# Optimization experiments

Hardware: AMD Instinct MI355X
Metric: run time of the kernel (lower is better)

Reference implementation:

```python
import jax, jax.numpy as jnp
import numpy as np

Q_HEADS = 16
KV_HEADS = 4
ROPE_THETA = 10000.0


def _rope(x, seq_len):
    # x: [B, S, H, D]; pairs are consecutive along D (view_as_complex semantics)
    D = x.shape[-1]
    inv_freq = 1.0 / (ROPE_THETA ** (jnp.arange(0, D, 2, dtype=jnp.float32) / D))
    freqs = jnp.arange(seq_len, dtype=jnp.float32)[:, None] * inv_freq  # [S, D/2]
    cos = jnp.cos(freqs)[None, :, None, :]
    sin = jnp.sin(freqs)[None, :, None, :]
    xr = x.reshape(x.shape[:-1] + (D // 2, 2))
    x0, x1 = xr[..., 0], xr[..., 1]
    out = jnp.stack([x0 * cos - x1 * sin, x0 * sin + x1 * cos], axis=-1)
    return out.reshape(x.shape)


def setup_inputs() -> dict:
    key = jax.random.key(0)
    ks = jax.random.split(key, 6)
    B, S, E = 1, 2048, 2048
    KV_DIM = KV_HEADS * (E // Q_HEADS)  # 512
    scale = 0.02
    return {
        "x": jax.random.normal(ks[0], (B, S, E), dtype=jnp.float32),
        "Wq": jax.random.normal(ks[1], (E, E), dtype=jnp.float32) * scale,
        "Wk": jax.random.normal(ks[2], (KV_DIM, E), dtype=jnp.float32) * scale,
        "Wv": jax.random.normal(ks[3], (KV_DIM, E), dtype=jnp.float32) * scale,
        "Wo": jax.random.normal(ks[4], (E, E), dtype=jnp.float32) * scale,
        "bo": jax.random.normal(ks[5], (E,), dtype=jnp.float32) * scale,
        "cache_keys": jnp.zeros((B, S, KV_HEADS, E // Q_HEADS), dtype=jnp.float32),
        "cache_value": jnp.zeros((B, S, KV_HEADS, E // Q_HEADS), dtype=jnp.float32),
        "start_pos": 0,
    }


def reference(x, Wq, Wk, Wv, Wo, bo, cache_keys, cache_value, start_pos):
    B, S, E = x.shape
    hd = E // Q_HEADS
    G = Q_HEADS // KV_HEADS  # queries per kv head

    xq = (x @ Wq.T).reshape(B, S, Q_HEADS, hd)
    xk = (x @ Wk.T).reshape(B, S, KV_HEADS, hd)
    xv = (x @ Wv.T).reshape(B, S, KV_HEADS, hd)

    # Original applies RoPE with positions 0..seq_len-1 for both q and k
    # (freq tensor is sliced [:seq_len] inside apply_rotry_position_embedding).
    xq = _rope(xq, S)
    xk = _rope(xk, S)

    # cache write at start_pos (static python int)
    cache_keys = jax.lax.dynamic_update_slice(cache_keys, xk, (0, start_pos, 0, 0))
    cache_value = jax.lax.dynamic_update_slice(cache_value, xv, (0, start_pos, 0, 0))
    total = start_pos + S
    k_full = cache_keys[:, :total]   # [B, T, KVH, hd]
    v_full = cache_value[:, :total]

    # repeat_interleave over the head axis == GQA expansion
    k = jnp.repeat(k_full, G, axis=2)  # [B, T, QH, hd]
    v = jnp.repeat(v_full, G, axis=2)

    scores = jnp.einsum("bshd,bthd->bhst", xq, k) / jnp.sqrt(jnp.float32(hd))
    causal = jnp.triu(jnp.ones((S, total), dtype=bool), k=1)  # [S, T]
    scores = jnp.where(causal[None, None, :, :], -jnp.inf, scores)
    weights = jax.nn.softmax(scores, axis=-1)
    out = jnp.einsum("bhst,bthd->bshd", weights, v).reshape(B, S, E)
    # dropout p=0.0 / eval mode -> identity
    return out @ Wo.T + bo
```

## Files before the change

### kernel.cpp

```cpp
#include <hip/hip_runtime.h>
#include <stdint.h>

typedef unsigned short u16;
typedef float  f32x4  __attribute__((ext_vector_type(4)));
typedef __bf16 bf16x8 __attribute__((ext_vector_type(8)));
typedef __bf16 bf16x4 __attribute__((ext_vector_type(4)));
typedef unsigned short u16x8 __attribute__((ext_vector_type(8)));
typedef unsigned short u16x4v __attribute__((ext_vector_type(4)));

#define S_LEN 2048
#define E_DIM 2048
#define HD    128
#define QH    16
#define KVH   4
#define KVD   512
#define NQKV  3072
#define QK_SCALE 0.08838834764831845f

#define AS1 __attribute__((address_space(1)))
#define AS3 __attribute__((address_space(3)))

__device__ __forceinline__ u16 f2bf(float f) {
  union { float f; uint32_t u; } v; v.f = f;
  return (u16)((v.u + 0x7FFFu + ((v.u >> 16) & 1u)) >> 16);
}

__global__ void cast_bf16_kernel(const float* __restrict__ in, u16* __restrict__ out) {
  int i = blockIdx.x * blockDim.x + threadIdx.x;
  float4 f = reinterpret_cast<const float4*>(in)[i];
  u16x4v o;
  o[0] = f2bf(f.x); o[1] = f2bf(f.y); o[2] = f2bf(f.z); o[3] = f2bf(f.w);
  reinterpret_cast<u16x4v*>(out)[i] = o;
}

template<bool BIAS>
__global__ __launch_bounds__(256) void gemm_bt_kernel(
    const u16* __restrict__ A, const u16* __restrict__ B,
    float* __restrict__ C, const float* __restrict__ bias,
    int M, int N, int K)
{
  __shared__ u16 As[2][128 * 64];
  __shared__ u16 Bs[2][128 * 64];

  const int tid  = threadIdx.x;
  const int lane = tid & 63;
  const int wid  = tid >> 6;
  const int wr   = (wid >> 1) * 64;
  const int wc   = (wid & 1) * 64;
  const int lr   = lane & 15;
  const int kg   = lane >> 4;

  const int bm = blockIdx.y * 128;
  const int bn = blockIdx.x * 128;

  f32x4 acc[4][4];
  #pragma unroll
  for (int r = 0; r < 4; ++r)
    #pragma unroll
    for (int c = 0; c < 4; ++c) acc[r][c] = (f32x4){0.f, 0.f, 0.f, 0.f};

  const int l8 = lane & 7;
  const int l3 = lane >> 3;
  const int schunk = l8 ^ l3;

  const u16* gA = A + (size_t)(bm + wid*32 + l3) * K + schunk * 8;
  const u16* gB = B + (size_t)(bn + wid*32 + l3) * K + schunk * 8;

  const int sw = lr & 7;

  auto stage = [&](int buf, int kt) {
    #pragma unroll
    for (int i = 0; i < 4; ++i) {
      __builtin_amdgcn_global_load_lds(
          (const AS1 void*)(gA + (size_t)i * 8 * K + kt),
          (AS3 void*)(&As[buf][wid*32*64 + i*8*64]), 16, 0, 0);
      __builtin_amdgcn_global_load_lds(
          (const AS1 void*)(gB + (size_t)i * 8 * K + kt),
          (AS3 void*)(&Bs[buf][wid*32*64 + i*8*64]), 16, 0, 0);
    }
  };

  stage(0, 0);
  __syncthreads();

  int cur = 0;
  for (int kt = 0; kt < K; kt += 64) {
    if (kt + 64 < K) stage(cur ^ 1, kt + 64);
    #pragma unroll
    for (int kk = 0; kk < 2; ++kk) {
      bf16x8 af[4], bfr[4];
      #pragma unroll
      for (int r = 0; r < 4; ++r)
        af[r] = *reinterpret_cast<const bf16x8*>(
            &As[cur][(wr + r*16 + lr)*64 + ((kk*4 + kg) ^ sw)*8]);
      #pragma unroll
      for (int c = 0; c < 4; ++c)
        bfr[c] = *reinterpret_cast<const bf16x8*>(
            &Bs[cur][(wc + c*16 + lr)*64 + ((kk*4 + kg) ^ sw)*8]);
      #pragma unroll
      for (int r = 0; r < 4; ++r)
        #pragma unroll
        for (int c = 0; c < 4; ++c)
          acc[r][c] = __builtin_amdgcn_mfma_f32_16x16x32_bf16(af[r], bfr[c], acc[r][c], 0, 0, 0);
    }
    __syncthreads();
    cur ^= 1;
  }

  const int crow = kg * 4;
  #pragma unroll
  for (int r = 0; r < 4; ++r) {
    #pragma unroll
    for (int c = 0; c < 4; ++c) {
      int gr = bm + wr + r*16 + crow;
      int gc = bn + wc + c*16 + lr;
      float badd = BIAS ? bias[gc] : 0.0f;
      #pragma unroll
      for (int reg = 0; reg < 4; ++reg)
        C[(size_t)(gr + reg)*N + gc] = acc[r][c][reg] + badd;
    }
  }
}

__global__ void rope_split_kernel(const float* __restrict__ qkv,
                                  u16* __restrict__ qb, u16* __restrict__ kb) {
  int idx = blockIdx.x * blockDim.x + threadIdx.x;
  int s  = idx / 1280;
  int cp = idx - s * 1280;
  int col = cp * 2;
  const float* src = qkv + (size_t)s * NQKV + col;
  float x0 = src[0], x1 = src[1];
  int p = (col & 127) >> 1;
  float inv = exp2f((float)p * (-13.287712379549449f / 64.0f));
  float ang = (float)s * inv;
  float sn, cs;
  sincosf(ang, &sn, &cs);
  float o0 = x0 * cs - x1 * sn;
  float o1 = x0 * sn + x1 * cs;
  if (col < E_DIM) {
    o0 *= QK_SCALE; o1 *= QK_SCALE;
    qb[(size_t)s * E_DIM + col]     = f2bf(o0);
    qb[(size_t)s * E_DIM + col + 1] = f2bf(o1);
  } else {
    kb[(size_t)s * KVD + (col - E_DIM)]     = f2bf(o0);
    kb[(size_t)s * KVD + (col - E_DIM) + 1] = f2bf(o1);
  }
}

__global__ void transpose_v_kernel(const float* __restrict__ qkv, u16* __restrict__ vT) {
  __shared__ float tile[32][33];
  const int sbase = blockIdx.x * 32;
  const int cbase = blockIdx.y * 32;
  const int tx = threadIdx.x;
  const int ty = threadIdx.y;
  #pragma unroll
  for (int i = 0; i < 32; i += 8)
    tile[ty + i][tx] = qkv[(size_t)(sbase + ty + i) * NQKV + (E_DIM + KVD) + cbase + tx];
  __syncthreads();
  #pragma unroll
  for (int i = 0; i < 32; i += 8)
    vT[(size_t)(cbase + ty + i) * S_LEN + sbase + tx] = f2bf(tile[tx][ty + i]);
}

__device__ __forceinline__ void attn_tile(
    int t, int qt, int wid, int lr, int kg,
    const bf16x8* qf, f32x4* o, float& mr, float& ls,
    const u16* ks, const u16* vts, u16* ps)
{
  const int sw = lr & 7;
  f32x4 st[4];
  #pragma unroll
  for (int c = 0; c < 4; ++c) st[c] = (f32x4){0.f, 0.f, 0.f, 0.f};
  __builtin_amdgcn_s_setprio(1);
  #pragma unroll
  for (int kk = 0; kk < 4; ++kk) {
    #pragma unroll
    for (int c = 0; c < 4; ++c) {
      bf16x8 kfr = *reinterpret_cast<const bf16x8*>(
          &ks[(c*16 + lr)*128 + ((kk*4 + kg) ^ sw)*8]);
      st[c] = __builtin_amdgcn_mfma_f32_16x16x32_bf16(kfr, qf[kk], st[c], 0, 0, 0);
    }
  }
  __builtin_amdgcn_s_setprio(0);
  if (t == qt) {
    #pragma unroll
    for (int c = 0; c < 4; ++c)
      #pragma unroll
      for (int reg = 0; reg < 4; ++reg)
        if (c*16 + kg*4 + reg > wid*16 + lr) st[c][reg] = -1e30f;
  }
  float cm[4];
  #pragma unroll
  for (int c = 0; c < 4; ++c)
    cm[c] = fmaxf(fmaxf(st[c][0], st[c][1]), fmaxf(st[c][2], st[c][3]));
  float pm = fmaxf(fmaxf(cm[0], cm[1]), fmaxf(cm[2], cm[3]));
  pm = fmaxf(pm, __shfl_xor(pm, 16));
  pm = fmaxf(pm, __shfl_xor(pm, 32));

  if (!__all(pm - mr <= 8.0f)) {
    float nm = fmaxf(mr, pm);
    float alpha = __expf(mr - nm);
    ls *= alpha;
    mr = nm;
    float ar[4];
    #pragma unroll
    for (int reg = 0; reg < 4; ++reg)
      ar[reg] = __shfl(alpha, kg*4 + reg);
    #pragma unroll
    for (int d = 0; d < 8; ++d)
      #pragma unroll
      for (int reg = 0; reg < 4; ++reg)
        o[d][reg] *= ar[reg];
  }

  float p[4][4];
  float csum[4];
  #pragma unroll
  for (int c = 0; c < 4; ++c) {
    #pragma unroll
    for (int reg = 0; reg < 4; ++reg)
      p[c][reg] = __expf(st[c][reg] - mr);
    csum[c] = (p[c][0] + p[c][1]) + (p[c][2] + p[c][3]);
  }
  float sum = (csum[0] + csum[1]) + (csum[2] + csum[3]);
  sum += __shfl_xor(sum, 16);
  sum += __shfl_xor(sum, 32);
  ls += sum;

  #pragma unroll
  for (int c = 0; c < 4; ++c) {
    bf16x4 pk;
    #pragma unroll
    for (int reg = 0; reg < 4; ++reg) pk[reg] = (__bf16)p[c][reg];
    *reinterpret_cast<bf16x4*>(&ps[lr*72 + c*16 + kg*4]) = pk;
  }
  __builtin_amdgcn_s_setprio(1);
  #pragma unroll
  for (int kk = 0; kk < 2; ++kk) {
    bf16x8 pa = *reinterpret_cast<const bf16x8*>(&ps[lr*72 + kk*32 + kg*8]);
    #pragma unroll
    for (int d = 0; d < 8; ++d) {
      bf16x8 vb = *reinterpret_cast<const bf16x8*>(
          &vts[(d*16 + lr)*64 + ((kk*4 + kg) ^ sw)*8]);
      o[d] = __builtin_amdgcn_mfma_f32_16x16x32_bf16(pa, vb, o[d], 0, 0, 0);
    }
  }
  __builtin_amdgcn_s_setprio(0);
}

__global__ __launch_bounds__(256, 2) void attn_kernel(
    const u16* __restrict__ Q, const u16* __restrict__ Kc,
    const u16* __restrict__ VT, u16* __restrict__ Out)
{
  __shared__ u16 Ks[2][64 * 128];
  __shared__ u16 VTs[2][128 * 64];
  __shared__ u16 Ps[4][16 * 72];

  const int x = blockIdx.x;
  int qt, h;
  if (x < 256) { qt = x & 31; h = x >> 5; }
  else         { int xp = x - 256; qt = 31 - (xp & 31); h = 8 + (xp >> 5); }
  const int kvh = h >> 2;
  const int tid  = threadIdx.x;
  const int lane = tid & 63;
  const int wid  = tid >> 6;
  const int lr   = lane & 15;
  const int kg   = lane >> 4;

  const int NT = qt + 1;

  bf16x8 qf[4];
  {
    const u16* qa = Q + (size_t)(qt*64 + wid*16 + lr) * E_DIM + h * HD + kg * 8;
    #pragma unroll
    for (int kk = 0; kk < 4; ++kk)
      qf[kk] = *reinterpret_cast<const bf16x8*>(qa + kk * 32);
  }

  f32x4 o[8];
  #pragma unroll
  for (int d = 0; d < 8; ++d) o[d] = (f32x4){0.f,0.f,0.f,0.f};
  float mr = -1e30f, ls = 0.f;

  u16x8 kreg[4], vreg[4];
  const u16* kbase = Kc + kvh * HD;
  const u16* vbase = VT + (size_t)(kvh * HD) * S_LEN;

  auto stage_load = [&](int t) {
    #pragma unroll
    for (int i = 0; i < 4; ++i) {
      int c = i * 256 + tid;
      kreg[i] = *reinterpret_cast<const u16x8*>(
          kbase + (size_t)(t*64 + (c >> 4)) * KVD + (c & 15) * 8);
      vreg[i] = *reinterpret_cast<const u16x8*>(
          vbase + (size_t)(c >> 3) * S_LEN + t*64 + (c & 7) * 8);
    }
  };
  auto stage_write = [&](int b) {
    #pragma unroll
    for (int i = 0; i < 4; ++i) {
      int c = i * 256 + tid;
      int kr = c >> 4, kc = c & 15;
      *reinterpret_cast<u16x8*>(&Ks[b][kr*128 + (kc ^ (kr & 7))*8]) = kreg[i];
      int vr = c >> 3, vc = c & 7;
      *reinterpret_cast<u16x8*>(&VTs[b][vr*64 + (vc ^ (vr & 7))*8]) = vreg[i];
    }
  };

  int p = 0;
  stage_load(0);
  stage_write(0);
  __syncthreads();

  for (int t = 0; t < NT; ++t) {
    if (t + 1 < NT) stage_load(t + 1);
    attn_tile(t, qt, wid, lr, kg, qf, o, mr, ls, Ks[p], VTs[p], Ps[wid]);
    if (t + 1 < NT) {
      stage_write(p ^ 1);
      __syncthreads();
      p ^= 1;
    }
  }

  {
    float inv = 1.0f / ls;
    float ivq[4];
    #pragma unroll
    for (int reg = 0; reg < 4; ++reg)
      ivq[reg] = __shfl(inv, kg*4 + reg);
    #pragma unroll
    for (int reg = 0; reg < 4; ++reg) {
      int grow = qt*64 + wid*16 + kg*4 + reg;
      #pragma unroll
      for (int d = 0; d < 8; ++d)
        Out[(size_t)grow * E_DIM + h * HD + d*16 + lr] =
            __builtin_bit_cast(u16, (__bf16)(o[d][reg] * ivq[reg]));
    }
  }
}

extern "C" void kernel_launch(void* const* d_in, const int* in_sizes, int n_in,
                              void* d_out, int out_size, void* d_ws, size_t ws_size,
                              hipStream_t stream)
{
  const float* x  = (const float*)d_in[0];
  const float* Wq = (const float*)d_in[1];
  const float* Wk = (const float*)d_in[2];
  const float* Wv = (const float*)d_in[3];
  const float* Wo = (const float*)d_in[4];
  const float* bo = (const float*)d_in[5];
  float* out = (float*)d_out;

  char* w = (char*)d_ws;
  u16*   xb   = (u16*)(w);
  u16*   Wcat = (u16*)(w + (8u  << 20));
  u16*   Wob  = (u16*)(w + (20u << 20));
  float* qkv  = (float*)(w + (28u << 20));
  u16*   qb   = (u16*)(w + (52u << 20));
  u16*   kb   = (u16*)(w + (60u << 20));
  u16*   vT   = (u16*)(w + (62u << 20));
  u16*   attn = (u16*)(w + (64u << 20));
  (void)ws_size; (void)in_sizes; (void)n_in; (void)out_size;

  cast_bf16_kernel<<<4096, 256, 0, stream>>>(x,  xb);
  cast_bf16_kernel<<<4096, 256, 0, stream>>>(Wq, Wcat);
  cast_bf16_kernel<<<1024, 256, 0, stream>>>(Wk, Wcat + (size_t)E_DIM * E_DIM);
  cast_bf16_kernel<<<1024, 256, 0, stream>>>(Wv, Wcat + (size_t)(E_DIM + KVD) * E_DIM);
  cast_bf16_kernel<<<4096, 256, 0, stream>>>(Wo, Wob);

  gemm_bt_kernel<false><<<dim3(NQKV/128, S_LEN/128), 256, 0, stream>>>(
      xb, Wcat, qkv, nullptr, S_LEN, NQKV, E_DIM);

  rope_split_kernel<<<(S_LEN * 1280) / 256, 256, 0, stream>>>(qkv, qb, kb);
  transpose_v_kernel<<<dim3(S_LEN/32, KVD/32), dim3(32, 8), 0, stream>>>(qkv, vT);

  attn_kernel<<<512, 256, 0, stream>>>(qb, kb, vT, attn);

  gemm_bt_kernel<true><<<dim3(E_DIM/128, S_LEN/128), 256, 0, stream>>>(
      attn, Wob, out, bo, S_LEN, E_DIM, E_DIM);
}
```

Before: 153.6 us.

## Fuse casts into one launch, use 512-thread GEMM, store QKV in bf16

Replaces the five separate fp32-to-bf16 cast launches with a single kernel that dispatches on index range. The GEMM now runs 8 waves per 128x128 tile, each wave computing a 64x32 sub-tile. The QKV projection writes bf16 instead of fp32, which halves its output traffic and the reads in the rope and V-transpose kernels. Rounding QKV to bf16 before RoPE adds a small precision loss, and the smaller per-wave tiles change the balance between LDS reads and MFMA work.

```diff
diff --git a/kernel.cpp b/kernel.cpp
--- a/kernel.cpp
+++ b/kernel.cpp
@@ -24,19 +24,33 @@
   union { float f; uint32_t u; } v; v.f = f;
   return (u16)((v.u + 0x7FFFu + ((v.u >> 16) & 1u)) >> 16);
 }
-
-__global__ void cast_bf16_kernel(const float* __restrict__ in, u16* __restrict__ out) {
+__device__ __forceinline__ float bf2f(u16 b) {
+  union { uint32_t u; float f; } v; v.u = ((uint32_t)b) << 16;
+  return v.f;
+}
+
+__global__ void cast_all_kernel(const float* __restrict__ x, const float* __restrict__ Wq,
+                                const float* __restrict__ Wk, const float* __restrict__ Wv,
+                                const float* __restrict__ Wo,
+                                u16* __restrict__ xb, u16* __restrict__ Wcat,
+                                u16* __restrict__ Wob) {
   int i = blockIdx.x * blockDim.x + threadIdx.x;
-  float4 f = reinterpret_cast<const float4*>(in)[i];
+  const float* src; u16* dst;
+  if (i < (1 << 20))                       { src = x  + (size_t)i * 4;  dst = xb + (size_t)i * 4; }
+  else if (i < (2 << 20))                  { size_t j = i - (1 << 20);  src = Wq + j * 4; dst = Wcat + j * 4; }
+  else if (i < (2 << 20) + (1 << 18))      { size_t j = i - (2 << 20);  src = Wk + j * 4; dst = Wcat + (size_t)E_DIM * E_DIM + j * 4; }
+  else if (i < (2 << 20) + (2 << 18))      { size_t j = i - (2 << 20) - (1 << 18); src = Wv + j * 4; dst = Wcat + (size_t)(E_DIM + KVD) * E_DIM + j * 4; }
+  else                                     { size_t j = i - (2 << 20) - (2 << 18); src = Wo + j * 4; dst = Wob + j * 4; }
+  float4 f = *reinterpret_cast<const float4*>(src);
   u16x4v o;
   o[0] = f2bf(f.x); o[1] = f2bf(f.y); o[2] = f2bf(f.z); o[3] = f2bf(f.w);
-  reinterpret_cast<u16x4v*>(out)[i] = o;
-}
-
-template<bool BIAS>
-__global__ __launch_bounds__(256) void gemm_bt_kernel(
+  *reinterpret_cast<u16x4v*>(dst) = o;
+}
+
+template<bool BIAS, bool OBF16>
+__global__ __launch_bounds__(512) void gemm_bt_kernel(
     const u16* __restrict__ A, const u16* __restrict__ B,
-    float* __restrict__ C, const float* __restrict__ bias,
+    void* __restrict__ Cv, const float* __restrict__ bias,
     int M, int N, int K)
 {
   __shared__ u16 As[2][128 * 64];
@@ -45,38 +59,36 @@
   const int tid  = threadIdx.x;
   const int lane = tid & 63;
   const int wid  = tid >> 6;
-  const int wr   = (wid >> 1) * 64;
-  const int wc   = (wid & 1) * 64;
+  const int wr   = (wid >> 2) * 64;
+  const int wc   = (wid & 3) * 32;
   const int lr   = lane & 15;
   const int kg   = lane >> 4;
+  const int sw   = lr & 7;
 
   const int bm = blockIdx.y * 128;
   const int bn = blockIdx.x * 128;
 
-  f32x4 acc[4][4];
+  f32x4 acc[4][2];
   #pragma unroll
   for (int r = 0; r < 4; ++r)
     #pragma unroll
-    for (int c = 0; c < 4; ++c) acc[r][c] = (f32x4){0.f, 0.f, 0.f, 0.f};
-
-  const int l8 = lane & 7;
-  const int l3 = lane >> 3;
-  const int schunk = l8 ^ l3;
-
-  const u16* gA = A + (size_t)(bm + wid*32 + l3) * K + schunk * 8;
-  const u16* gB = B + (size_t)(bn + wid*32 + l3) * K + schunk * 8;
-
-  const int sw = lr & 7;
+    for (int c = 0; c < 2; ++c) acc[r][c] = (f32x4){0.f, 0.f, 0.f, 0.f};
+
+  const int srow   = wid * 8 + (lane >> 3);
+  const int schunk = (lane & 7) ^ (lane >> 3);
+
+  const u16* gA = A + (size_t)(bm + srow) * K + schunk * 8;
+  const u16* gB = B + (size_t)(bn + srow) * K + schunk * 8;
 
   auto stage = [&](int buf, int kt) {
     #pragma unroll
-    for (int i = 0; i < 4; ++i) {
+    for (int i = 0; i < 2; ++i) {
       __builtin_amdgcn_global_load_lds(
-          (const AS1 void*)(gA + (size_t)i * 8 * K + kt),
-          (AS3 void*)(&As[buf][wid*32*64 + i*8*64]), 16, 0, 0);
+          (const AS1 void*)(gA + (size_t)i * 64 * K + kt),
+          (AS3 void*)(&As[buf][(wid*8 + i*64) * 64]), 16, 0, 0);
       __builtin_amdgcn_global_load_lds(
-          (const AS1 void*)(gB + (size_t)i * 8 * K + kt),
-          (AS3 void*)(&Bs[buf][wid*32*64 + i*8*64]), 16, 0, 0);
+          (const AS1 void*)(gB + (size_t)i * 64 * K + kt),
+          (AS3 void*)(&Bs[buf][(wid*8 + i*64) * 64]), 16, 0, 0);
     }
   };
 
@@ -88,19 +100,19 @@
     if (kt + 64 < K) stage(cur ^ 1, kt + 64);
     #pragma unroll
     for (int kk = 0; kk < 2; ++kk) {
-      bf16x8 af[4], bfr[4];
+      bf16x8 af[4], bfr[2];
       #pragma unroll
       for (int r = 0; r < 4; ++r)
         af[r] = *reinterpret_cast<const bf16x8*>(
             &As[cur][(wr + r*16 + lr)*64 + ((kk*4 + kg) ^ sw)*8]);
       #pragma unroll
-      for (int c = 0; c < 4; ++c)
+      for (int c = 0; c < 2; ++c)
         bfr[c] = *reinterpret_cast<const bf16x8*>(
             &Bs[cur][(wc + c*16 + lr)*64 + ((kk*4 + kg) ^ sw)*8]);
       #pragma unroll
       for (int r = 0; r < 4; ++r)
         #pragma unroll
-        for (int c = 0; c < 4; ++c)
+        for (int c = 0; c < 2; ++c)
           acc[r][c] = __builtin_amdgcn_mfma_f32_16x16x32_bf16(af[r], bfr[c], acc[r][c], 0, 0, 0);
     }
     __syncthreads();
@@ -111,25 +123,30 @@
   #pragma unroll
   for (int r = 0; r < 4; ++r) {
     #pragma unroll
-    for (int c = 0; c < 4; ++c) {
+    for (int c = 0; c < 2; ++c) {
       int gr = bm + wr + r*16 + crow;
       int gc = bn + wc + c*16 + lr;
       float badd = BIAS ? bias[gc] : 0.0f;
       #pragma unroll
-      for (int reg = 0; reg < 4; ++reg)
-        C[(size_t)(gr + reg)*N + gc] = acc[r][c][reg] + badd;
-    }
-  }
-}
-
-__global__ void rope_split_kernel(const float* __restrict__ qkv,
+      for (int reg = 0; reg < 4; ++reg) {
+        float v = acc[r][c][reg] + badd;
+        if constexpr (OBF16)
+          ((u16*)Cv)[(size_t)(gr + reg)*N + gc] = f2bf(v);
+        else
+          ((float*)Cv)[(size_t)(gr + reg)*N + gc] = v;
+      }
+    }
+  }
+}
+
+__global__ void rope_split_kernel(const u16* __restrict__ qkv,
                                   u16* __restrict__ qb, u16* __restrict__ kb) {
   int idx = blockIdx.x * blockDim.x + threadIdx.x;
   int s  = idx / 1280;
   int cp = idx - s * 1280;
   int col = cp * 2;
-  const float* src = qkv + (size_t)s * NQKV + col;
-  float x0 = src[0], x1 = src[1];
+  const u16* src = qkv + (size_t)s * NQKV + col;
+  float x0 = bf2f(src[0]), x1 = bf2f(src[1]);
   int p = (col & 127) >> 1;
   float inv = exp2f((float)p * (-13.287712379549449f / 64.0f));
   float ang = (float)s * inv;
@@ -147,8 +164,8 @@
   }
 }
 
-__global__ void transpose_v_kernel(const float* __restrict__ qkv, u16* __restrict__ vT) {
-  __shared__ float tile[32][33];
+__global__ void transpose_v_kernel(const u16* __restrict__ qkv, u16* __restrict__ vT) {
+  __shared__ u16 tile[32][33];
   const int sbase = blockIdx.x * 32;
   const int cbase = blockIdx.y * 32;
   const int tx = threadIdx.x;
@@ -159,7 +176,7 @@
   __syncthreads();
   #pragma unroll
   for (int i = 0; i < 32; i += 8)
-    vT[(size_t)(cbase + ty + i) * S_LEN + sbase + tx] = f2bf(tile[tx][ty + i]);
+    vT[(size_t)(cbase + ty + i) * S_LEN + sbase + tx] = tile[tx][ty + i];
 }
 
 __device__ __forceinline__ void attn_tile(
@@ -355,20 +372,16 @@
   u16*   xb   = (u16*)(w);
   u16*   Wcat = (u16*)(w + (8u  << 20));
   u16*   Wob  = (u16*)(w + (20u << 20));
-  float* qkv  = (float*)(w + (28u << 20));
+  u16*   qkv  = (u16*)(w + (28u << 20));
   u16*   qb   = (u16*)(w + (52u << 20));
   u16*   kb   = (u16*)(w + (60u << 20));
   u16*   vT   = (u16*)(w + (62u << 20));
   u16*   attn = (u16*)(w + (64u << 20));
   (void)ws_size; (void)in_sizes; (void)n_in; (void)out_size;
 
-  cast_bf16_kernel<<<4096, 256, 0, stream>>>(x,  xb);
-  cast_bf16_kernel<<<4096, 256, 0, stream>>>(Wq, Wcat);
-  cast_bf16_kernel<<<1024, 256, 0, stream>>>(Wk, Wcat + (size_t)E_DIM * E_DIM);
-  cast_bf16_kernel<<<1024, 256, 0, stream>>>(Wv, Wcat + (size_t)(E_DIM + KVD) * E_DIM);
-  cast_bf16_kernel<<<4096, 256, 0, stream>>>(Wo, Wob);
-
-  gemm_bt_kernel<false><<<dim3(NQKV/128, S_LEN/128), 256, 0, stream>>>(
+  cast_all_kernel<<<14336, 256, 0, stream>>>(x, Wq, Wk, Wv, Wo, xb, Wcat, Wob);
+
+  gemm_bt_kernel<false, true><<<dim3(NQKV/128, S_LEN/128), 512, 0, stream>>>(
       xb, Wcat, qkv, nullptr, S_LEN, NQKV, E_DIM);
 
   rope_split_kernel<<<(S_LEN * 1280) / 256, 256, 0, stream>>>(qkv, qb, kb);
@@ -376,6 +389,6 @@
 
   attn_kernel<<<512, 256, 0, stream>>>(qb, kb, vT, attn);
 
-  gemm_bt_kernel<true><<<dim3(E_DIM/128, S_LEN/128), 256, 0, stream>>>(
+  gemm_bt_kernel<true, false><<<dim3(E_DIM/128, S_LEN/128), 512, 0, stream>>>(
       attn, Wob, out, bo, S_LEN, E_DIM, E_DIM);
 }
```

New measurement: 139.9 us. -8.9%, faster.
